# Performance work log

Hardware: AMD Instinct MI355X
Metric: run time of the kernel (lower is better)

The kernel has to match this reference:

```python
import jax, jax.numpy as jnp
import numpy as np

B, S, D_MODEL, H = 4, 1025, 1024, 16
DEPTH = D_MODEL // H
LEAKY_ALPHA = 0.2  # tf.nn.leaky_relu default
NEG_INF = -1e9


def _dense_params(key, d_in, d_out):
    kw, kb = jax.random.split(key)
    W = jax.random.normal(kw, (d_in, d_out), dtype=jnp.float32) * 0.02
    b = jnp.zeros((d_out,), dtype=jnp.float32)
    return W, b


def setup_inputs() -> dict:
    key = jax.random.key(0)
    ks = jax.random.split(key, 13)
    inp = {
        'q': jax.random.normal(ks[0], (B, S, D_MODEL), dtype=jnp.float32),
        'k': jax.random.normal(ks[1], (B, S, D_MODEL), dtype=jnp.float32),
        'v': jax.random.normal(ks[2], (B, S - 1, D_MODEL), dtype=jnp.float32),
        'e': jax.random.normal(ks[3], (B, S, D_MODEL), dtype=jnp.float32),
        'mask': jax.random.randint(ks[4], (B, S - 1, S - 1), 0, 2).astype(jnp.float32),
    }
    names = ['wq', 'wq2', 'wq3', 'wk', 'wk2', 'wk3', 'wv', 'wo']
    for i, nm in enumerate(names):
        W, b = _dense_params(ks[5 + i], D_MODEL, D_MODEL)
        inp['W' + nm] = W
        inp['b' + nm] = b
    return inp


def _split_heads(x):
    # (B, S, d_model) -> (B, H, S, depth)
    b, s, _ = x.shape
    return x.reshape(b, s, H, DEPTH).transpose(0, 2, 1, 3)


def reference(q, k, v, e, mask,
              Wwq, bwq, Wwq2, bwq2, Wwq3, bwq3,
              Wwk, bwk, Wwk2, bwk2, Wwk3, bwk3,
              Wwv, bwv, Wwo, bwo):
    # Q/K pre-projections mixed with edge/extra features e, leaky_relu(alpha=0.2)
    qp = jax.nn.leaky_relu(q @ Wwq + bwq + e @ Wwq2 + bwq2, LEAKY_ALPHA) @ Wwq3 + bwq3
    kp = jax.nn.leaky_relu(k @ Wwk + bwk + e @ Wwk2 + bwk2, LEAKY_ALPHA) @ Wwk3 + bwk3
    vp = v @ Wwv + bwv

    qh = _split_heads(qp)  # (B,H,S,depth)
    kh = _split_heads(kp)  # (B,H,S,depth)
    vh = _split_heads(vp)  # (B,H,S-1,depth)

    # scores: (B,H,S,S) then slice rows 1: and cols :-1 -> (B,H,S-1,S-1)
    scores = jnp.einsum('bhqd,bhkd->bhqk', qh, kh)
    sliced = scores[:, :, 1:, :-1]
    scale = 1.0 / jnp.sqrt(jnp.asarray(DEPTH, dtype=sliced.dtype))
    nl_qk = jax.nn.relu(sliced * scale) + mask[:, None, :, :] * NEG_INF
    att_weights = jax.nn.softmax(nl_qk, axis=-1)  # (B,H,S-1,S-1)

    out = jnp.einsum('bhqk,bhkd->bhqd', att_weights, vh)  # (B,H,S-1,depth)
    out = out.transpose(0, 2, 1, 3).reshape(out.shape[0], -1, D_MODEL)
    output = out @ Wwo + bwo  # (B,S-1,d_model)
    return output, att_weights
```

## Files before the change

### kernel.cpp

```cpp
#include <hip/hip_runtime.h>

#define DM 1024
typedef unsigned short u16;
typedef __attribute__((ext_vector_type(8))) short short8;
typedef __attribute__((ext_vector_type(4))) float f32x4;

__device__ __forceinline__ float4 ldg4(const float* p) {
    return *reinterpret_cast<const float4*>(p);
}

__device__ __forceinline__ void split2(float x, u16& hi, u16& lo) {
    unsigned u = __float_as_uint(x);
    hi = (u16)(u >> 16);
    float hif = __uint_as_float(u & 0xffff0000u);
    lo = (u16)(__float_as_uint(x - hif) >> 16);
}

__device__ __forceinline__ u16 bf16rn(float x) {
    unsigned u = __float_as_uint(x);
    return (u16)((u + 0x7fffu + ((u >> 16) & 1u)) >> 16);
}

__device__ __forceinline__ int swzc(int row, int col) {
    return (col & ~63) | (((((col >> 3) & 7) ^ (row & 7))) << 3) | (col & 7);
}

__device__ __forceinline__ void gl_lds16(const u16* g, u16* l) {
    __builtin_amdgcn_global_load_lds(
        (const __attribute__((address_space(1))) void*)g,
        (__attribute__((address_space(3))) void*)l, 16, 0, 0);
}

struct PJob { const float* src; int astride, aoff; u16* dh; u16* dl; };
struct PJobs { PJob j[5]; };

__global__ __launch_bounds__(256) void prep_k(PJobs js) {
    const PJob J = js.j[blockIdx.x >> 12];
    const int row = blockIdx.x & 4095;
    const int t = threadIdx.x;
    const size_t srow = (size_t)(row >> 10) * J.astride + (row & 1023) + J.aoff;
    float4 v = ldg4(J.src + srow * DM + t * 4);
    u16 h[4], l[4];
    split2(v.x, h[0], l[0]); split2(v.y, h[1], l[1]);
    split2(v.z, h[2], l[2]); split2(v.w, h[3], l[3]);
    ushort4 h4 = {h[0], h[1], h[2], h[3]};
    ushort4 l4 = {l[0], l[1], l[2], l[3]};
    const int c = swzc(row, t * 4);
    *reinterpret_cast<ushort4*>(J.dh + (size_t)row * DM + c) = h4;
    *reinterpret_cast<ushort4*>(J.dl + (size_t)row * DM + c) = l4;
}

struct WPack {
    const float* in[8];
    u16* hi[8];
    u16* lo[8];
};

__global__ __launch_bounds__(256) void convw_k(WPack p) {
    __shared__ float T[32][33];
    const int w = blockIdx.y;
    const int tr = blockIdx.x >> 5, tc = blockIdx.x & 31;
    const int t = threadIdx.x;
    {
        int lr = t >> 3, c4 = t & 7;
        float4 v = ldg4(p.in[w] + (size_t)(tr * 32 + lr) * DM + tc * 32 + c4 * 4);
        T[lr][c4 * 4 + 0] = v.x; T[lr][c4 * 4 + 1] = v.y;
        T[lr][c4 * 4 + 2] = v.z; T[lr][c4 * 4 + 3] = v.w;
    }
    __syncthreads();
    const int n = tc * 32 + (t >> 3);
    const int kb = tr * 32 + (t & 7) * 4;
    ushort4 h4, l4;
    u16 hh, ll;
    split2(T[(t & 7) * 4 + 0][t >> 3], hh, ll); h4.x = hh; l4.x = ll;
    split2(T[(t & 7) * 4 + 1][t >> 3], hh, ll); h4.y = hh; l4.y = ll;
    split2(T[(t & 7) * 4 + 2][t >> 3], hh, ll); h4.z = hh; l4.z = ll;
    split2(T[(t & 7) * 4 + 3][t >> 3], hh, ll); h4.w = hh; l4.w = ll;
    const int c = swzc(n, kb);
    *reinterpret_cast<ushort4*>(p.hi[w] + (size_t)n * DM + c) = h4;
    *reinterpret_cast<ushort4*>(p.lo[w] + (size_t)n * DM + c) = l4;
}

struct GJob {
    const u16 *Ah, *Al, *A2h, *A2l;
    const u16 *Bh, *Bl, *B2h, *B2l;
    const float *b1, *b2;
    float* Cf; u16 *Ch; u16 *Cl;
    int nt, act, outsplit, dualk;
};
struct GJobs { GJob j[3]; };

__global__ __launch_bounds__(256) void gemm6(GJobs js) {
    extern __shared__ u16 lds[];
    const GJob J = js.j[blockIdx.x >> 8];
    const int lb = blockIdx.x & 255;
    const int bid = ((lb & 7) << 5) | (lb >> 3);
    const int t = threadIdx.x;
    const int bm = bid >> 3, bn = bid & 7;
    const int lane = t & 63, w = t >> 6;
    const int wm = w >> 1, wn = w & 1;
    const int fr = lane & 15, fq = lane >> 4;

    const size_t ga = ((size_t)(bm * 128 + w * 32 + (lane >> 3))) * DM + (lane & 7) * 8;
    const size_t gb = ((size_t)(bn * 128 + w * 32 + (lane >> 3))) * DM + (lane & 7) * 8;

    f32x4 acc[4][4];
    #pragma unroll
    for (int i = 0; i < 4; ++i)
        #pragma unroll
        for (int j = 0; j < 4; ++j)
            acc[i][j] = (f32x4){0.f, 0.f, 0.f, 0.f};

    auto STAGE = [&](int kt, int buf) {
        const bool second = J.dualk && (kt >= 16);
        const int ekt = J.dualk ? (kt & 15) : kt;
        const u16* pAh = second ? J.A2h : J.Ah;
        const u16* pAl = second ? J.A2l : J.Al;
        const u16* pBh = second ? J.B2h : J.Bh;
        const u16* pBl = second ? J.B2l : J.Bl;
        const size_t ka = ga + ekt * 64;
        const size_t kb = gb + ekt * 64;
        u16* base = lds + buf * 32768;
        #pragma unroll
        for (int i = 0; i < 4; ++i) {
            const int lo = w * 2048 + i * 512;
            const size_t go = (size_t)i * 8 * DM;
            gl_lds16(pAh + ka + go, base +         lo);
            gl_lds16(pAl + ka + go, base +  8192 + lo);
            gl_lds16(pBh + kb + go, base + 16384 + lo);
            gl_lds16(pBl + kb + go, base + 24576 + lo);
        }
    };

    auto COMPUTE = [&](int buf) {
        const u16* base = lds + buf * 32768;
        #pragma unroll
        for (int kk = 0; kk < 2; ++kk) {
            short8 ah[4], al[4];
            #pragma unroll
            for (int mi = 0; mi < 4; ++mi) {
                const int row = wm * 64 + mi * 16 + fr;
                const int off = row * 64 + (((kk * 4 + fq) ^ (row & 7)) << 3);
                ah[mi] = *reinterpret_cast<const short8*>(base + off);
                al[mi] = *reinterpret_cast<const short8*>(base + 8192 + off);
            }
            #pragma unroll
            for (int nj = 0; nj < 4; ++nj) {
                const int rb = wn * 64 + nj * 16 + fr;
                const int off = rb * 64 + (((kk * 4 + fq) ^ (rb & 7)) << 3);
                short8 bh = *reinterpret_cast<const short8*>(base + 16384 + off);
                short8 bl = *reinterpret_cast<const short8*>(base + 24576 + off);
                #pragma unroll
                for (int mi = 0; mi < 4; ++mi) {
                    acc[mi][nj] = __builtin_amdgcn_mfma_f32_16x16x32_bf16(ah[mi], bh, acc[mi][nj], 0, 0, 0);
                    acc[mi][nj] = __builtin_amdgcn_mfma_f32_16x16x32_bf16(ah[mi], bl, acc[mi][nj], 0, 0, 0);
                    acc[mi][nj] = __builtin_amdgcn_mfma_f32_16x16x32_bf16(al[mi], bh, acc[mi][nj], 0, 0, 0);
                }
            }
        }
    };

    const int NT = J.nt;
    STAGE(0, 0);
    __syncthreads();
    for (int kt = 0; kt < NT; ++kt) {
        if (kt + 1 < NT) STAGE(kt + 1, (kt + 1) & 1);
        COMPUTE(kt & 1);
        __syncthreads();
    }

    #pragma unroll
    for (int nj = 0; nj < 4; ++nj) {
        const int col = bn * 128 + wn * 64 + nj * 16 + fr;
        float bv = J.b1[col];
        if (J.dualk) bv += J.b2[col];
        #pragma unroll
        for (int mi = 0; mi < 4; ++mi) {
            const int row0 = bm * 128 + wm * 64 + mi * 16 + fq * 4;
            #pragma unroll
            for (int rr = 0; rr < 4; ++rr) {
                float x = acc[mi][nj][rr] + bv;
                if (J.act) x = (x >= 0.f) ? x : 0.2f * x;
                const int row = row0 + rr;
                if (J.outsplit) {
                    u16 hh, ll;
                    split2(x, hh, ll);
                    const size_t off = (size_t)row * DM + swzc(row, col);
                    J.Ch[off] = hh;
                    J.Cl[off] = ll;
                } else {
                    J.Cf[(size_t)row * DM + col] = x;
                }
            }
        }
    }
}

__global__ __launch_bounds__(256) void attn2(
    const float* __restrict__ qp, const float* __restrict__ kp,
    const float* __restrict__ vp, const float* __restrict__ mask,
    float* __restrict__ att, u16* __restrict__ omidH, u16* __restrict__ omidL,
    float* __restrict__ rsg)
{
    extern __shared__ u16 sm16[];
    u16* Qh  = sm16;
    u16* Ql  = sm16 + 4608;
    u16* Kh  = sm16 + 9216;
    u16* Kl  = sm16 + 18432;
    float* Sf = (float*)(sm16 + 9216);
    u16* Vth = sm16 + 9216;
    u16* Vtl = sm16 + 17920;
    u16* Ps  = sm16 + 27648;
    float* rs = (float*)(sm16 + 36352);

    const int t = threadIdx.x;
    const int lane = t & 63, w = t >> 6;
    const int wm = w >> 1, wn = w & 1;
    const int fr = lane & 15, fq = lane >> 4;
    const int blk = blockIdx.x;
    const int qt = blk & 15, hh = (blk >> 4) & 15, b = blk >> 8;
    const int q0 = qt * 64;

    const size_t qbase  = ((size_t)b * 1024 + q0) * DM + hh * 64;
    const size_t kvbase = ((size_t)b * 1024) * DM + hh * 64;
    const size_t mbase  = ((size_t)b) << 20;
    const size_t abase  = ((size_t)(b * 16 + hh)) << 20;

    #pragma unroll
    for (int l = 0; l < 4; ++l) {
        int f = t + l * 256;
        int r = f >> 4, dq = f & 15;
        float4 v = ldg4(qp + qbase + (size_t)r * DM + dq * 4);
        u16 hi, lo; ushort4 h4, l4;
        split2(v.x, hi, lo); h4.x = hi; l4.x = lo;
        split2(v.y, hi, lo); h4.y = hi; l4.y = lo;
        split2(v.z, hi, lo); h4.z = hi; l4.z = lo;
        split2(v.w, hi, lo); h4.w = hi; l4.w = lo;
        *reinterpret_cast<ushort4*>(Qh + r * 72 + dq * 4) = h4;
        *reinterpret_cast<ushort4*>(Ql + r * 72 + dq * 4) = l4;
    }

    f32x4 pv[2][2];
    #pragma unroll
    for (int i = 0; i < 2; ++i)
        #pragma unroll
        for (int j = 0; j < 2; ++j)
            pv[i][j] = (f32x4){0.f, 0.f, 0.f, 0.f};
    float rpart[8] = {};

    float4 kreg[8];
    #pragma unroll
    for (int l = 0; l < 8; ++l) {
        int f = t + l * 256;
        int r = f >> 4, dq = f & 15;
        kreg[l] = ldg4(kp + kvbase + (size_t)r * DM + dq * 4);
    }

    for (int kt2 = 0; kt2 < 8; ++kt2) {
        const int kb = kt2 * 128;
        __syncthreads();

        #pragma unroll
        for (int l = 0; l < 8; ++l) {
            int f = t + l * 256;
            int r = f >> 4, dq = f & 15;
            float4 v = kreg[l];
            u16 hi, lo; ushort4 h4, l4;
            split2(v.x, hi, lo); h4.x = hi; l4.x = lo;
            split2(v.y, hi, lo); h4.y = hi; l4.y = lo;
            split2(v.z, hi, lo); h4.z = hi; l4.z = lo;
            split2(v.w, hi, lo); h4.w = hi; l4.w = lo;
            *reinterpret_cast<ushort4*>(Kh + r * 72 + dq * 4) = h4;
            *reinterpret_cast<ushort4*>(Kl + r * 72 + dq * 4) = l4;
        }
        __syncthreads();

        float4 vreg[8], mreg[8];
        {
            const int k_ = t >> 1, hd = t & 1;
            const float* src = vp + kvbase + (size_t)(kb + k_) * DM + hd * 32;
            #pragma unroll
            for (int c = 0; c < 8; ++c) vreg[c] = ldg4(src + c * 4);
        }
        #pragma unroll
        for (int l = 0; l < 8; ++l) {
            const int row = (t >> 5) + l * 8;
            mreg[l] = ldg4(mask + mbase + (size_t)(q0 + row) * 1024 + kb + (t & 31) * 4);
        }

        f32x4 accs[2][4];
        #pragma unroll
        for (int i = 0; i < 2; ++i)
            #pragma unroll
            for (int j = 0; j < 4; ++j)
                accs[i][j] = (f32x4){0.f, 0.f, 0.f, 0.f};
        #pragma unroll
        for (int kk = 0; kk < 2; ++kk) {
            short8 qh_[2], ql_[2];
            #pragma unroll
            for (int mi = 0; mi < 2; ++mi) {
                const int off = (wm * 32 + mi * 16 + fr) * 72 + kk * 32 + fq * 8;
                qh_[mi] = *reinterpret_cast<const short8*>(Qh + off);
                ql_[mi] = *reinterpret_cast<const short8*>(Ql + off);
            }
            #pragma unroll
            for (int nj = 0; nj < 4; ++nj) {
                const int off = (wn * 64 + nj * 16 + fr) * 72 + kk * 32 + fq * 8;
                short8 kh_ = *reinterpret_cast<const short8*>(Kh + off);
                short8 kl_ = *reinterpret_cast<const short8*>(Kl + off);
                #pragma unroll
                for (int mi = 0; mi < 2; ++mi) {
                    accs[mi][nj] = __builtin_amdgcn_mfma_f32_16x16x32_bf16(qh_[mi], kh_, accs[mi][nj], 0, 0, 0);
                    accs[mi][nj] = __builtin_amdgcn_mfma_f32_16x16x32_bf16(qh_[mi], kl_, accs[mi][nj], 0, 0, 0);
                    accs[mi][nj] = __builtin_amdgcn_mfma_f32_16x16x32_bf16(ql_[mi], kh_, accs[mi][nj], 0, 0, 0);
                }
            }
        }
        __syncthreads();

        #pragma unroll
        for (int mi = 0; mi < 2; ++mi)
            #pragma unroll
            for (int rr = 0; rr < 4; ++rr) {
                const int qrow = wm * 32 + mi * 16 + fq * 4 + rr;
                #pragma unroll
                for (int nj = 0; nj < 4; ++nj)
                    Sf[qrow * 132 + wn * 64 + nj * 16 + fr] = accs[mi][nj][rr];
            }
        __syncthreads();

        #pragma unroll
        for (int l = 0; l < 8; ++l) {
            const int row = (t >> 5) + l * 8;
            const int gq = q0 + row;
            float4 sv = *reinterpret_cast<const float4*>(Sf + row * 132 + (t & 31) * 4);
            float e[4];
            float s4[4] = {sv.x, sv.y, sv.z, sv.w};
            float m4[4] = {mreg[l].x, mreg[l].y, mreg[l].z, mreg[l].w};
            #pragma unroll
            for (int u = 0; u < 4; ++u) {
                float x = fmaxf(s4[u] * 0.125f, 0.f);
                x = fmaf(m4[u], -1.0e9f, x);
                e[u] = __expf(x);
                rpart[l] += e[u];
            }
            float4 ev = {e[0], e[1], e[2], e[3]};
            *reinterpret_cast<float4*>(att + abase + (size_t)gq * 1024 + kb + (t & 31) * 4) = ev;
            ushort4 pp = {bf16rn(e[0]), bf16rn(e[1]), bf16rn(e[2]), bf16rn(e[3])};
            *reinterpret_cast<ushort4*>(Ps + row * 136 + (t & 31) * 4) = pp;
        }
        __syncthreads();

        {
            const int k_ = t >> 1, hd = t & 1;
            #pragma unroll
            for (int c = 0; c < 8; ++c) {
                float4 v = vreg[c];
                const int d0 = hd * 32 + c * 4;
                u16 hi, lo;
                split2(v.x, hi, lo); Vth[(d0+0)*136 + k_] = hi; Vtl[(d0+0)*136 + k_] = lo;
                split2(v.y, hi, lo); Vth[(d0+1)*136 + k_] = hi; Vtl[(d0+1)*136 + k_] = lo;
                split2(v.z, hi, lo); Vth[(d0+2)*136 + k_] = hi; Vtl[(d0+2)*136 + k_] = lo;
                split2(v.w, hi, lo); Vth[(d0+3)*136 + k_] = hi; Vtl[(d0+3)*136 + k_] = lo;
            }
        }
        __syncthreads();

        {
            const int nkb = (kt2 < 7 ? kt2 + 1 : 7) * 128;
            #pragma unroll
            for (int l = 0; l < 8; ++l) {
                int f = t + l * 256;
                int r = f >> 4, dq = f & 15;
                kreg[l] = ldg4(kp + kvbase + (size_t)(nkb + r) * DM + dq * 4);
            }
        }

        #pragma unroll
        for (int kk = 0; kk < 4; ++kk) {
            short8 pa[2];
            #pragma unroll
            for (int mi = 0; mi < 2; ++mi)
                pa[mi] = *reinterpret_cast<const short8*>(
                    Ps + (wm * 32 + mi * 16 + fr) * 136 + kk * 32 + fq * 8);
            #pragma unroll
            for (int nj = 0; nj < 2; ++nj) {
                const int off = (wn * 32 + nj * 16 + fr) * 136 + kk * 32 + fq * 8;
                short8 vh_ = *reinterpret_cast<const short8*>(Vth + off);
                short8 vl_ = *reinterpret_cast<const short8*>(Vtl + off);
                #pragma unroll
                for (int mi = 0; mi < 2; ++mi) {
                    pv[mi][nj] = __builtin_amdgcn_mfma_f32_16x16x32_bf16(pa[mi], vh_, pv[mi][nj], 0, 0, 0);
                    pv[mi][nj] = __builtin_amdgcn_mfma_f32_16x16x32_bf16(pa[mi], vl_, pv[mi][nj], 0, 0, 0);
                }
            }
        }
    }

    #pragma unroll
    for (int l = 0; l < 8; ++l) {
        float v = rpart[l];
        v += __shfl_xor(v, 1);
        v += __shfl_xor(v, 2);
        v += __shfl_xor(v, 4);
        v += __shfl_xor(v, 8);
        v += __shfl_xor(v, 16);
        if ((t & 31) == 0) rs[(t >> 5) + l * 8] = v;
    }
    __syncthreads();
    if (t < 64) {
        float iv = 1.f / rs[t];
        rs[t] = iv;
        rsg[(size_t)(b * 16 + hh) * 1024 + q0 + t] = iv;
    }
    __syncthreads();

    #pragma unroll
    for (int mi = 0; mi < 2; ++mi) {
        #pragma unroll
        for (int rr = 0; rr < 4; ++rr) {
            const int qrow = wm * 32 + mi * 16 + fq * 4 + rr;
            const float iv = rs[qrow];
            const size_t grow = (size_t)b * 1024 + q0 + qrow;
            #pragma unroll
            for (int nj = 0; nj < 2; ++nj) {
                const int d = hh * 64 + wn * 32 + nj * 16 + fr;
                float x = pv[mi][nj][rr] * iv;
                u16 hi, lo;
                split2(x, hi, lo);
                const size_t off = grow * DM + swzc(qrow, d);
                omidH[off] = hi;
                omidL[off] = lo;
            }
        }
    }
}

__global__ __launch_bounds__(256) void norm_k(
    float* __restrict__ att, const float* __restrict__ rsg)
{
    const size_t total = (size_t)67108864 / 4;
    for (size_t i = (size_t)blockIdx.x * 256 + threadIdx.x; i < total;
         i += (size_t)gridDim.x * 256) {
        float4 v = reinterpret_cast<float4*>(att)[i];
        float s = rsg[i >> 8];
        v.x *= s; v.y *= s; v.z *= s; v.w *= s;
        reinterpret_cast<float4*>(att)[i] = v;
    }
}

extern "C" void kernel_launch(void* const* d_in, const int* in_sizes, int n_in,
                              void* d_out, int out_size, void* d_ws, size_t ws_size,
                              hipStream_t stream)
{
    const float* q    = (const float*)d_in[0];
    const float* k    = (const float*)d_in[1];
    const float* v    = (const float*)d_in[2];
    const float* e    = (const float*)d_in[3];
    const float* mask = (const float*)d_in[4];
    const float* bq   = (const float*)d_in[6];
    const float* bq2  = (const float*)d_in[8];
    const float* bq3  = (const float*)d_in[10];
    const float* bk   = (const float*)d_in[12];
    const float* bk2  = (const float*)d_in[14];
    const float* bk3  = (const float*)d_in[16];
    const float* bv   = (const float*)d_in[18];
    const float* bo   = (const float*)d_in[20];

    float* out = (float*)d_out;
    float* att = out + (size_t)4096 * 1024;

    u16* WT = (u16*)d_ws;
    const size_t WSZ = 1048576;
    const size_t NA = (size_t)4096 * 1024;
    float* qp   = (float*)(WT + 16 * WSZ);
    float* kp   = qp + NA;
    float* vpp  = kp + NA;
    u16* omidH  = (u16*)(vpp + NA);
    u16* omidL  = omidH + NA;
    float* rsg  = (float*)(omidL + NA);

    u16* AR   = (u16*)att;
    u16* QspH = AR;            u16* QspL = QspH + NA;
    u16* E1H  = QspL + NA;     u16* E1L  = E1H + NA;
    u16* KspH = E1L + NA;      u16* KspL = KspH + NA;
    u16* E0H  = KspL + NA;     u16* E0L  = E0H + NA;
    u16* VsH  = E0L + NA;      u16* VsL  = VsH + NA;
    u16* tQH  = VsL + NA;      u16* tQL  = tQH + NA;
    u16* tKH  = tQL + NA;      u16* tKL  = tKH + NA;

    PJobs pj;
    pj.j[0] = PJob{q, 1025, 1, QspH, QspL};
    pj.j[1] = PJob{e, 1025, 1, E1H, E1L};
    pj.j[2] = PJob{k, 1025, 0, KspH, KspL};
    pj.j[3] = PJob{e, 1025, 0, E0H, E0L};
    pj.j[4] = PJob{v, 1024, 0, VsH, VsL};
    prep_k<<<dim3(5 * 4096), 256, 0, stream>>>(pj);

    WPack wp;
    #pragma unroll
    for (int i = 0; i < 8; ++i) {
        wp.in[i] = (const float*)d_in[5 + 2 * i];
        wp.hi[i] = WT + (size_t)i * 2 * WSZ;
        wp.lo[i] = WT + (size_t)i * 2 * WSZ + WSZ;
    }
    convw_k<<<dim3(1024, 8), 256, 0, stream>>>(wp);

    hipFuncSetAttribute((const void*)gemm6, hipFuncAttributeMaxDynamicSharedMemorySize, 131072);

    GJobs JA;
    JA.j[0] = GJob{QspH, QspL, E1H, E1L, wp.hi[0], wp.lo[0], wp.hi[1], wp.lo[1],
                   bq, bq2, nullptr, tQH, tQL, 32, 1, 1, 1};
    JA.j[1] = GJob{KspH, KspL, E0H, E0L, wp.hi[3], wp.lo[3], wp.hi[4], wp.lo[4],
                   bk, bk2, nullptr, tKH, tKL, 32, 1, 1, 1};
    JA.j[2] = GJob{VsH, VsL, nullptr, nullptr, wp.hi[6], wp.lo[6], nullptr, nullptr,
                   bv, nullptr, vpp, nullptr, nullptr, 16, 0, 0, 0};
    gemm6<<<dim3(768), 256, 131072, stream>>>(JA);

    GJobs JB;
    JB.j[0] = GJob{tQH, tQL, nullptr, nullptr, wp.hi[2], wp.lo[2], nullptr, nullptr,
                   bq3, nullptr, qp, nullptr, nullptr, 16, 0, 0, 0};
    JB.j[1] = GJob{tKH, tKL, nullptr, nullptr, wp.hi[5], wp.lo[5], nullptr, nullptr,
                   bk3, nullptr, kp, nullptr, nullptr, 16, 0, 0, 0};
    JB.j[2] = JB.j[0];
    gemm6<<<dim3(512), 256, 131072, stream>>>(JB);

    const int smemA = 72960;
    hipFuncSetAttribute((const void*)attn2, hipFuncAttributeMaxDynamicSharedMemorySize, smemA);
    attn2<<<dim3(1024), 256, smemA, stream>>>(qp, kp, vpp, mask, att, omidH, omidL, rsg);

    norm_k<<<dim3(16384), 256, 0, stream>>>(att, rsg);

    GJobs JC;
    JC.j[0] = GJob{omidH, omidL, nullptr, nullptr, wp.hi[7], wp.lo[7], nullptr, nullptr,
                   bo, nullptr, out, nullptr, nullptr, 16, 0, 0, 0};
    JC.j[1] = JC.j[0];
    JC.j[2] = JC.j[0];
    gemm6<<<dim3(256), 256, 131072, stream>>>(JC);
}
```

Baseline: 823.6 us.

## Split attention into row-sum pass, compact mask to bytes, retile GEMMs to 256x256

Attention becomes two kernels. The first recomputes QK scores to get the softmax row sums. The second writes already-normalised attention weights directly, which removes the separate normalisation pass that read and rewrote the whole attention tensor. The float mask is compacted to a uint8 buffer, cutting mask traffic, and masked entries are zeroed instead of adding -1e9. The split-bf16 GEMM moves to 256x256 tiles with 512 threads, a 32-wide K step and a matching new swizzle. The price is far fewer GEMM blocks per launch, as few as 64 for the output projection, plus a second QK computation.

```diff
diff --git a/kernel.cpp b/kernel.cpp
--- a/kernel.cpp
+++ b/kernel.cpp
@@ -21,8 +21,8 @@
     return (u16)((u + 0x7fffu + ((u >> 16) & 1u)) >> 16);
 }
 
-__device__ __forceinline__ int swzc(int row, int col) {
-    return (col & ~63) | (((((col >> 3) & 7) ^ (row & 7))) << 3) | (col & 7);
+__device__ __forceinline__ int swz32(int row, int col) {
+    return (col & ~31) | ((((col >> 3) & 3) ^ ((row >> 1) & 3)) << 3) | (col & 7);
 }
 
 __device__ __forceinline__ void gl_lds16(const u16* g, u16* l) {
@@ -45,7 +45,7 @@
     split2(v.z, h[2], l[2]); split2(v.w, h[3], l[3]);
     ushort4 h4 = {h[0], h[1], h[2], h[3]};
     ushort4 l4 = {l[0], l[1], l[2], l[3]};
-    const int c = swzc(row, t * 4);
+    const int c = swz32(row, t * 4);
     *reinterpret_cast<ushort4*>(J.dh + (size_t)row * DM + c) = h4;
     *reinterpret_cast<ushort4*>(J.dl + (size_t)row * DM + c) = l4;
 }
@@ -76,9 +76,19 @@
     split2(T[(t & 7) * 4 + 1][t >> 3], hh, ll); h4.y = hh; l4.y = ll;
     split2(T[(t & 7) * 4 + 2][t >> 3], hh, ll); h4.z = hh; l4.z = ll;
     split2(T[(t & 7) * 4 + 3][t >> 3], hh, ll); h4.w = hh; l4.w = ll;
-    const int c = swzc(n, kb);
+    const int c = swz32(n, kb);
     *reinterpret_cast<ushort4*>(p.hi[w] + (size_t)n * DM + c) = h4;
     *reinterpret_cast<ushort4*>(p.lo[w] + (size_t)n * DM + c) = l4;
+}
+
+__global__ __launch_bounds__(256) void mprep_k(
+    const float* __restrict__ mask, unsigned char* __restrict__ m8)
+{
+    const size_t i = ((size_t)blockIdx.x * 256 + threadIdx.x) * 4;
+    float4 v = ldg4(mask + i);
+    uchar4 o = {(unsigned char)(v.x != 0.f), (unsigned char)(v.y != 0.f),
+                (unsigned char)(v.z != 0.f), (unsigned char)(v.w != 0.f)};
+    *reinterpret_cast<uchar4*>(m8 + i) = o;
 }
 
 struct GJob {
@@ -90,72 +100,71 @@
 };
 struct GJobs { GJob j[3]; };
 
-__global__ __launch_bounds__(256) void gemm6(GJobs js) {
+__global__ __launch_bounds__(512) void gemm7(GJobs js) {
     extern __shared__ u16 lds[];
-    const GJob J = js.j[blockIdx.x >> 8];
-    const int lb = blockIdx.x & 255;
-    const int bid = ((lb & 7) << 5) | (lb >> 3);
+    const GJob J = js.j[blockIdx.x >> 6];
+    const int bid = blockIdx.x & 63;
     const int t = threadIdx.x;
-    const int bm = bid >> 3, bn = bid & 7;
+    const int bm = bid >> 2, bn = bid & 3;
     const int lane = t & 63, w = t >> 6;
-    const int wm = w >> 1, wn = w & 1;
+    const int wm = w >> 2, wn = w & 3;
     const int fr = lane & 15, fq = lane >> 4;
 
-    const size_t ga = ((size_t)(bm * 128 + w * 32 + (lane >> 3))) * DM + (lane & 7) * 8;
-    const size_t gb = ((size_t)(bn * 128 + w * 32 + (lane >> 3))) * DM + (lane & 7) * 8;
-
-    f32x4 acc[4][4];
-    #pragma unroll
-    for (int i = 0; i < 4; ++i)
+    const int sr = lane >> 2;
+    const int sg = (lane & 3) * 8;
+    const size_t gA0 = (size_t)(bm * 256 + w * 32 + sr) * DM + sg;
+    const size_t gA1 = gA0 + (size_t)16 * DM;
+    const size_t gB0 = (size_t)(bn * 256 + w * 32 + sr) * DM + sg;
+    const size_t gB1 = gB0 + (size_t)16 * DM;
+    const int l0 = (w * 32) * 32;
+
+    f32x4 acc[8][4];
+    #pragma unroll
+    for (int i = 0; i < 8; ++i)
         #pragma unroll
         for (int j = 0; j < 4; ++j)
             acc[i][j] = (f32x4){0.f, 0.f, 0.f, 0.f};
 
     auto STAGE = [&](int kt, int buf) {
-        const bool second = J.dualk && (kt >= 16);
-        const int ekt = J.dualk ? (kt & 15) : kt;
+        const bool second = J.dualk && (kt >= 32);
+        const int ekt = J.dualk ? (kt & 31) : kt;
         const u16* pAh = second ? J.A2h : J.Ah;
         const u16* pAl = second ? J.A2l : J.Al;
         const u16* pBh = second ? J.B2h : J.Bh;
         const u16* pBl = second ? J.B2l : J.Bl;
-        const size_t ka = ga + ekt * 64;
-        const size_t kb = gb + ekt * 64;
+        const int ko = ekt * 32;
         u16* base = lds + buf * 32768;
-        #pragma unroll
-        for (int i = 0; i < 4; ++i) {
-            const int lo = w * 2048 + i * 512;
-            const size_t go = (size_t)i * 8 * DM;
-            gl_lds16(pAh + ka + go, base +         lo);
-            gl_lds16(pAl + ka + go, base +  8192 + lo);
-            gl_lds16(pBh + kb + go, base + 16384 + lo);
-            gl_lds16(pBl + kb + go, base + 24576 + lo);
-        }
+        gl_lds16(pAh + gA0 + ko, base +         l0);
+        gl_lds16(pAh + gA1 + ko, base +         l0 + 512);
+        gl_lds16(pAl + gA0 + ko, base +  8192 + l0);
+        gl_lds16(pAl + gA1 + ko, base +  8192 + l0 + 512);
+        gl_lds16(pBh + gB0 + ko, base + 16384 + l0);
+        gl_lds16(pBh + gB1 + ko, base + 16384 + l0 + 512);
+        gl_lds16(pBl + gB0 + ko, base + 24576 + l0);
+        gl_lds16(pBl + gB1 + ko, base + 24576 + l0 + 512);
     };
 
     auto COMPUTE = [&](int buf) {
         const u16* base = lds + buf * 32768;
-        #pragma unroll
-        for (int kk = 0; kk < 2; ++kk) {
-            short8 ah[4], al[4];
-            #pragma unroll
-            for (int mi = 0; mi < 4; ++mi) {
-                const int row = wm * 64 + mi * 16 + fr;
-                const int off = row * 64 + (((kk * 4 + fq) ^ (row & 7)) << 3);
-                ah[mi] = *reinterpret_cast<const short8*>(base + off);
-                al[mi] = *reinterpret_cast<const short8*>(base + 8192 + off);
-            }
-            #pragma unroll
-            for (int nj = 0; nj < 4; ++nj) {
-                const int rb = wn * 64 + nj * 16 + fr;
-                const int off = rb * 64 + (((kk * 4 + fq) ^ (rb & 7)) << 3);
-                short8 bh = *reinterpret_cast<const short8*>(base + 16384 + off);
-                short8 bl = *reinterpret_cast<const short8*>(base + 24576 + off);
-                #pragma unroll
-                for (int mi = 0; mi < 4; ++mi) {
-                    acc[mi][nj] = __builtin_amdgcn_mfma_f32_16x16x32_bf16(ah[mi], bh, acc[mi][nj], 0, 0, 0);
-                    acc[mi][nj] = __builtin_amdgcn_mfma_f32_16x16x32_bf16(ah[mi], bl, acc[mi][nj], 0, 0, 0);
-                    acc[mi][nj] = __builtin_amdgcn_mfma_f32_16x16x32_bf16(al[mi], bh, acc[mi][nj], 0, 0, 0);
-                }
+        short8 ah[8], al[8];
+        #pragma unroll
+        for (int mi = 0; mi < 8; ++mi) {
+            const int row = wm * 128 + mi * 16 + fr;
+            const int off = row * 32 + ((fq ^ ((row >> 1) & 3)) << 3);
+            ah[mi] = *reinterpret_cast<const short8*>(base + off);
+            al[mi] = *reinterpret_cast<const short8*>(base + 8192 + off);
+        }
+        #pragma unroll
+        for (int nj = 0; nj < 4; ++nj) {
+            const int col = wn * 64 + nj * 16 + fr;
+            const int off = col * 32 + ((fq ^ ((col >> 1) & 3)) << 3);
+            short8 bh = *reinterpret_cast<const short8*>(base + 16384 + off);
+            short8 bl = *reinterpret_cast<const short8*>(base + 24576 + off);
+            #pragma unroll
+            for (int mi = 0; mi < 8; ++mi) {
+                acc[mi][nj] = __builtin_amdgcn_mfma_f32_16x16x32_bf16(ah[mi], bh, acc[mi][nj], 0, 0, 0);
+                acc[mi][nj] = __builtin_amdgcn_mfma_f32_16x16x32_bf16(ah[mi], bl, acc[mi][nj], 0, 0, 0);
+                acc[mi][nj] = __builtin_amdgcn_mfma_f32_16x16x32_bf16(al[mi], bh, acc[mi][nj], 0, 0, 0);
             }
         }
     };
@@ -171,12 +180,12 @@
 
     #pragma unroll
     for (int nj = 0; nj < 4; ++nj) {
-        const int col = bn * 128 + wn * 64 + nj * 16 + fr;
+        const int col = bn * 256 + wn * 64 + nj * 16 + fr;
         float bv = J.b1[col];
         if (J.dualk) bv += J.b2[col];
         #pragma unroll
-        for (int mi = 0; mi < 4; ++mi) {
-            const int row0 = bm * 128 + wm * 64 + mi * 16 + fq * 4;
+        for (int mi = 0; mi < 8; ++mi) {
+            const int row0 = bm * 256 + wm * 128 + mi * 16 + fq * 4;
             #pragma unroll
             for (int rr = 0; rr < 4; ++rr) {
                 float x = acc[mi][nj][rr] + bv;
@@ -185,7 +194,7 @@
                 if (J.outsplit) {
                     u16 hh, ll;
                     split2(x, hh, ll);
-                    const size_t off = (size_t)row * DM + swzc(row, col);
+                    const size_t off = (size_t)row * DM + swz32(row, col);
                     J.Ch[off] = hh;
                     J.Cl[off] = ll;
                 } else {
@@ -196,11 +205,143 @@
     }
 }
 
-__global__ __launch_bounds__(256) void attn2(
+__global__ __launch_bounds__(256) void attn_a(
     const float* __restrict__ qp, const float* __restrict__ kp,
-    const float* __restrict__ vp, const float* __restrict__ mask,
+    const unsigned char* __restrict__ m8, float* __restrict__ rsg)
+{
+    __shared__ u16 Qh[64 * 72], Ql[64 * 72], Kh[128 * 72], Kl[128 * 72];
+    __shared__ float rs[2][64];
+
+    const int t = threadIdx.x;
+    const int lane = t & 63, w = t >> 6;
+    const int wm = w >> 1, wn = w & 1;
+    const int fr = lane & 15, fq = lane >> 4;
+    const int blk = blockIdx.x;
+    const int qt = blk & 15, hh = (blk >> 4) & 15, b = blk >> 8;
+    const int q0 = qt * 64;
+
+    const size_t qbase  = ((size_t)b * 1024 + q0) * DM + hh * 64;
+    const size_t kvbase = ((size_t)b * 1024) * DM + hh * 64;
+    const size_t mb8    = ((size_t)b) << 20;
+
+    #pragma unroll
+    for (int l = 0; l < 4; ++l) {
+        int f = t + l * 256;
+        int r = f >> 4, dq = f & 15;
+        float4 v = ldg4(qp + qbase + (size_t)r * DM + dq * 4);
+        u16 hi, lo; ushort4 h4, l4;
+        split2(v.x, hi, lo); h4.x = hi; l4.x = lo;
+        split2(v.y, hi, lo); h4.y = hi; l4.y = lo;
+        split2(v.z, hi, lo); h4.z = hi; l4.z = lo;
+        split2(v.w, hi, lo); h4.w = hi; l4.w = lo;
+        *reinterpret_cast<ushort4*>(Qh + r * 72 + dq * 4) = h4;
+        *reinterpret_cast<ushort4*>(Ql + r * 72 + dq * 4) = l4;
+    }
+
+    float rpart[2][4] = {};
+
+    float4 kreg[8];
+    #pragma unroll
+    for (int l = 0; l < 8; ++l) {
+        int f = t + l * 256;
+        int r = f >> 4, dq = f & 15;
+        kreg[l] = ldg4(kp + kvbase + (size_t)r * DM + dq * 4);
+    }
+
+    for (int kt2 = 0; kt2 < 8; ++kt2) {
+        const int kb = kt2 * 128;
+        __syncthreads();
+        #pragma unroll
+        for (int l = 0; l < 8; ++l) {
+            int f = t + l * 256;
+            int r = f >> 4, dq = f & 15;
+            float4 v = kreg[l];
+            u16 hi, lo; ushort4 h4, l4;
+            split2(v.x, hi, lo); h4.x = hi; l4.x = lo;
+            split2(v.y, hi, lo); h4.y = hi; l4.y = lo;
+            split2(v.z, hi, lo); h4.z = hi; l4.z = lo;
+            split2(v.w, hi, lo); h4.w = hi; l4.w = lo;
+            *reinterpret_cast<ushort4*>(Kh + r * 72 + dq * 4) = h4;
+            *reinterpret_cast<ushort4*>(Kl + r * 72 + dq * 4) = l4;
+        }
+        __syncthreads();
+
+        {
+            const int nkb = (kt2 < 7 ? kt2 + 1 : 7) * 128;
+            #pragma unroll
+            for (int l = 0; l < 8; ++l) {
+                int f = t + l * 256;
+                int r = f >> 4, dq = f & 15;
+                kreg[l] = ldg4(kp + kvbase + (size_t)(nkb + r) * DM + dq * 4);
+            }
+        }
+
+        f32x4 accs[2][4];
+        #pragma unroll
+        for (int i = 0; i < 2; ++i)
+            #pragma unroll
+            for (int j = 0; j < 4; ++j)
+                accs[i][j] = (f32x4){0.f, 0.f, 0.f, 0.f};
+        #pragma unroll
+        for (int kk = 0; kk < 2; ++kk) {
+            short8 qh_[2], ql_[2];
+            #pragma unroll
+            for (int mi = 0; mi < 2; ++mi) {
+                const int off = (wm * 32 + mi * 16 + fr) * 72 + kk * 32 + fq * 8;
+                qh_[mi] = *reinterpret_cast<const short8*>(Qh + off);
+                ql_[mi] = *reinterpret_cast<const short8*>(Ql + off);
+            }
+            #pragma unroll
+            for (int nj = 0; nj < 4; ++nj) {
+                const int off = (wn * 64 + nj * 16 + fr) * 72 + kk * 32 + fq * 8;
+                short8 kh_ = *reinterpret_cast<const short8*>(Kh + off);
+                short8 kl_ = *reinterpret_cast<const short8*>(Kl + off);
+                #pragma unroll
+                for (int mi = 0; mi < 2; ++mi) {
+                    accs[mi][nj] = __builtin_amdgcn_mfma_f32_16x16x32_bf16(qh_[mi], kh_, accs[mi][nj], 0, 0, 0);
+                    accs[mi][nj] = __builtin_amdgcn_mfma_f32_16x16x32_bf16(qh_[mi], kl_, accs[mi][nj], 0, 0, 0);
+                    accs[mi][nj] = __builtin_amdgcn_mfma_f32_16x16x32_bf16(ql_[mi], kh_, accs[mi][nj], 0, 0, 0);
+                }
+            }
+        }
+
+        #pragma unroll
+        for (int mi = 0; mi < 2; ++mi)
+            #pragma unroll
+            for (int rr = 0; rr < 4; ++rr) {
+                const int gq = q0 + wm * 32 + mi * 16 + fq * 4 + rr;
+                const size_t mrow = mb8 + (size_t)gq * 1024 + kb;
+                #pragma unroll
+                for (int nj = 0; nj < 4; ++nj) {
+                    const int kc = wn * 64 + nj * 16 + fr;
+                    unsigned char m = m8[mrow + kc];
+                    float x = fmaxf(accs[mi][nj][rr] * 0.125f, 0.f);
+                    if (!m) rpart[mi][rr] += __expf(x);
+                }
+            }
+    }
+
+    #pragma unroll
+    for (int mi = 0; mi < 2; ++mi)
+        #pragma unroll
+        for (int rr = 0; rr < 4; ++rr) {
+            float v = rpart[mi][rr];
+            v += __shfl_xor(v, 1);
+            v += __shfl_xor(v, 2);
+            v += __shfl_xor(v, 4);
+            v += __shfl_xor(v, 8);
+            if (fr == 0) rs[wn][wm * 32 + mi * 16 + fq * 4 + rr] = v;
+        }
+    __syncthreads();
+    if (t < 64)
+        rsg[(size_t)(b * 16 + hh) * 1024 + q0 + t] = 1.f / (rs[0][t] + rs[1][t]);
+}
+
+__global__ __launch_bounds__(256) void attn_b(
+    const float* __restrict__ qp, const float* __restrict__ kp,
+    const float* __restrict__ vp, const unsigned char* __restrict__ m8,
     float* __restrict__ att, u16* __restrict__ omidH, u16* __restrict__ omidL,
-    float* __restrict__ rsg)
+    const float* __restrict__ rsg)
 {
     extern __shared__ u16 sm16[];
     u16* Qh  = sm16;
@@ -223,8 +364,10 @@
 
     const size_t qbase  = ((size_t)b * 1024 + q0) * DM + hh * 64;
     const size_t kvbase = ((size_t)b * 1024) * DM + hh * 64;
-    const size_t mbase  = ((size_t)b) << 20;
+    const size_t mb8    = ((size_t)b) << 20;
     const size_t abase  = ((size_t)(b * 16 + hh)) << 20;
+
+    if (t < 64) rs[t] = rsg[(size_t)(b * 16 + hh) * 1024 + q0 + t];
 
     #pragma unroll
     for (int l = 0; l < 4; ++l) {
@@ -246,7 +389,6 @@
         #pragma unroll
         for (int j = 0; j < 2; ++j)
             pv[i][j] = (f32x4){0.f, 0.f, 0.f, 0.f};
-    float rpart[8] = {};
 
     float4 kreg[8];
     #pragma unroll
@@ -275,17 +417,12 @@
         }
         __syncthreads();
 
-        float4 vreg[8], mreg[8];
+        float4 vreg[8];
         {
             const int k_ = t >> 1, hd = t & 1;
             const float* src = vp + kvbase + (size_t)(kb + k_) * DM + hd * 32;
             #pragma unroll
             for (int c = 0; c < 8; ++c) vreg[c] = ldg4(src + c * 4);
-        }
-        #pragma unroll
-        for (int l = 0; l < 8; ++l) {
-            const int row = (t >> 5) + l * 8;
-            mreg[l] = ldg4(mask + mbase + (size_t)(q0 + row) * 1024 + kb + (t & 31) * 4);
         }
 
         f32x4 accs[2][4];
@@ -334,15 +471,16 @@
             const int row = (t >> 5) + l * 8;
             const int gq = q0 + row;
             float4 sv = *reinterpret_cast<const float4*>(Sf + row * 132 + (t & 31) * 4);
+            uchar4 mq = *reinterpret_cast<const uchar4*>(
+                m8 + mb8 + (size_t)gq * 1024 + kb + (t & 31) * 4);
+            const float iv = rs[row];
             float e[4];
             float s4[4] = {sv.x, sv.y, sv.z, sv.w};
-            float m4[4] = {mreg[l].x, mreg[l].y, mreg[l].z, mreg[l].w};
+            unsigned char m4[4] = {mq.x, mq.y, mq.z, mq.w};
             #pragma unroll
             for (int u = 0; u < 4; ++u) {
                 float x = fmaxf(s4[u] * 0.125f, 0.f);
-                x = fmaf(m4[u], -1.0e9f, x);
-                e[u] = __expf(x);
-                rpart[l] += e[u];
+                e[u] = m4[u] ? 0.f : iv * __expf(x);
             }
             float4 ev = {e[0], e[1], e[2], e[3]};
             *reinterpret_cast<float4*>(att + abase + (size_t)gq * 1024 + kb + (t & 31) * 4) = ev;
@@ -398,54 +536,21 @@
     }
 
     #pragma unroll
-    for (int l = 0; l < 8; ++l) {
-        float v = rpart[l];
-        v += __shfl_xor(v, 1);
-        v += __shfl_xor(v, 2);
-        v += __shfl_xor(v, 4);
-        v += __shfl_xor(v, 8);
-        v += __shfl_xor(v, 16);
-        if ((t & 31) == 0) rs[(t >> 5) + l * 8] = v;
-    }
-    __syncthreads();
-    if (t < 64) {
-        float iv = 1.f / rs[t];
-        rs[t] = iv;
-        rsg[(size_t)(b * 16 + hh) * 1024 + q0 + t] = iv;
-    }
-    __syncthreads();
-
-    #pragma unroll
     for (int mi = 0; mi < 2; ++mi) {
         #pragma unroll
         for (int rr = 0; rr < 4; ++rr) {
             const int qrow = wm * 32 + mi * 16 + fq * 4 + rr;
-            const float iv = rs[qrow];
             const size_t grow = (size_t)b * 1024 + q0 + qrow;
             #pragma unroll
             for (int nj = 0; nj < 2; ++nj) {
                 const int d = hh * 64 + wn * 32 + nj * 16 + fr;
-                float x = pv[mi][nj][rr] * iv;
                 u16 hi, lo;
-                split2(x, hi, lo);
-                const size_t off = grow * DM + swzc(qrow, d);
+                split2(pv[mi][nj][rr], hi, lo);
+                const size_t off = grow * DM + swz32(qrow, d);
                 omidH[off] = hi;
                 omidL[off] = lo;
             }
         }
-    }
-}
-
-__global__ __launch_bounds__(256) void norm_k(
-    float* __restrict__ att, const float* __restrict__ rsg)
-{
-    const size_t total = (size_t)67108864 / 4;
-    for (size_t i = (size_t)blockIdx.x * 256 + threadIdx.x; i < total;
-         i += (size_t)gridDim.x * 256) {
-        float4 v = reinterpret_cast<float4*>(att)[i];
-        float s = rsg[i >> 8];
-        v.x *= s; v.y *= s; v.z *= s; v.w *= s;
-        reinterpret_cast<float4*>(att)[i] = v;
     }
 }
 
@@ -479,6 +584,7 @@
     u16* omidH  = (u16*)(vpp + NA);
     u16* omidL  = omidH + NA;
     float* rsg  = (float*)(omidL + NA);
+    unsigned char* m8 = (unsigned char*)WT;
 
     u16* AR   = (u16*)att;
     u16* QspH = AR;            u16* QspL = QspH + NA;
@@ -506,35 +612,37 @@
     }
     convw_k<<<dim3(1024, 8), 256, 0, stream>>>(wp);
 
-    hipFuncSetAttribute((const void*)gemm6, hipFuncAttributeMaxDynamicSharedMemorySize, 131072);
+    hipFuncSetAttribute((const void*)gemm7, hipFuncAttributeMaxDynamicSharedMemorySize, 131072);
 
     GJobs JA;
     JA.j[0] = GJob{QspH, QspL, E1H, E1L, wp.hi[0], wp.lo[0], wp.hi[1], wp.lo[1],
-                   bq, bq2, nullptr, tQH, tQL, 32, 1, 1, 1};
+                   bq, bq2, nullptr, tQH, tQL, 64, 1, 1, 1};
     JA.j[1] = GJob{KspH, KspL, E0H, E0L, wp.hi[3], wp.lo[3], wp.hi[4], wp.lo[4],
-                   bk, bk2, nullptr, tKH, tKL, 32, 1, 1, 1};
+                   bk, bk2, nullptr, tKH, tKL, 64, 1, 1, 1};
     JA.j[2] = GJob{VsH, VsL, nullptr, nullptr, wp.hi[6], wp.lo[6], nullptr, nullptr,
-                   bv, nullptr, vpp, nullptr, nullptr, 16, 0, 0, 0};
-    gemm6<<<dim3(768), 256, 131072, stream>>>(JA);
+                   bv, nullptr, vpp, nullptr, nullptr, 32, 0, 0, 0};
+    gemm7<<<dim3(192), 512, 131072, stream>>>(JA);
+
+    mprep_k<<<dim3(4096), 256, 0, stream>>>(mask, m8);
 
     GJobs JB;
     JB.j[0] = GJob{tQH, tQL, nullptr, nullptr, wp.hi[2], wp.lo[2], nullptr, nullptr,
-                   bq3, nullptr, qp, nullptr, nullptr, 16, 0, 0, 0};
+                   bq3, nullptr, qp, nullptr, nullptr, 32, 0, 0, 0};
     JB.j[1] = GJob{tKH, tKL, nullptr, nullptr, wp.hi[5], wp.lo[5], nullptr, nullptr,
-                   bk3, nullptr, kp, nullptr, nullptr, 16, 0, 0, 0};
+                   bk3, nullptr, kp, nullptr, nullptr, 32, 0, 0, 0};
     JB.j[2] = JB.j[0];
-    gemm6<<<dim3(512), 256, 131072, stream>>>(JB);
+    gemm7<<<dim3(128), 512, 131072, stream>>>(JB);
+
+    attn_a<<<dim3(1024), 256, 0, stream>>>(qp, kp, m8, rsg);
 
     const int smemA = 72960;
-    hipFuncSetAttribute((const void*)attn2, hipFuncAttributeMaxDynamicSharedMemorySize, smemA);
-    attn2<<<dim3(1024), 256, smemA, stream>>>(qp, kp, vpp, mask, att, omidH, omidL, rsg);
-
-    norm_k<<<dim3(16384), 256, 0, stream>>>(att, rsg);
+    hipFuncSetAttribute((const void*)attn_b, hipFuncAttributeMaxDynamicSharedMemorySize, smemA);
+    attn_b<<<dim3(1024), 256, smemA, stream>>>(qp, kp, vpp, m8, att, omidH, omidL, rsg);
 
     GJobs JC;
     JC.j[0] = GJob{omidH, omidL, nullptr, nullptr, wp.hi[7], wp.lo[7], nullptr, nullptr,
-                   bo, nullptr, out, nullptr, nullptr, 16, 0, 0, 0};
+                   bo, nullptr, out, nullptr, nullptr, 32, 0, 0, 0};
     JC.j[1] = JC.j[0];
     JC.j[2] = JC.j[0];
-    gemm6<<<dim3(256), 256, 131072, stream>>>(JC);
-}
+    gemm7<<<dim3(64), 512, 131072, stream>>>(JC);
+}
```

After: 925.3 us. 12.3% more time.
